# Kernel tuning notes

Hardware: AMD Instinct MI355X
Metric: run time of the kernel (lower is better)

Reference implementation:

```python
import jax, jax.numpy as jnp
import numpy as np

B, T, D = 2, 2048, 512
H, L, DFF, W = 8, 4, 2048, 256
DH = D // H  # 64
EPS = 1e-5


def layer_norm(x, g, b):
    mu = jnp.mean(x, axis=-1, keepdims=True)
    var = jnp.var(x, axis=-1, keepdims=True)
    return (x - mu) * jax.lax.rsqrt(var + EPS) * g + b


def setup_inputs() -> dict:
    key = jax.random.key(0)
    ks = jax.random.split(key, 8)
    s = 0.02
    inp = {
        "tokens": jax.random.normal(ks[0], (B, T, D), jnp.float32),
        "Wq": jax.random.normal(ks[1], (L, D, D), jnp.float32) * s,
        "Wk": jax.random.normal(ks[2], (L, D, D), jnp.float32) * s,
        "Wv": jax.random.normal(ks[3], (L, D, D), jnp.float32) * s,
        "Wo": jax.random.normal(ks[4], (L, D, D), jnp.float32) * s,
        "bq": jnp.zeros((L, D), jnp.float32),
        "bk": jnp.zeros((L, D), jnp.float32),
        "bv": jnp.zeros((L, D), jnp.float32),
        "bo": jnp.zeros((L, D), jnp.float32),
        "W1": jax.random.normal(ks[5], (L, D, DFF), jnp.float32) * s,
        "b1": jnp.zeros((L, DFF), jnp.float32),
        "W2": jax.random.normal(ks[6], (L, DFF, D), jnp.float32) * s,
        "b2": jnp.zeros((L, D), jnp.float32),
        "g1": jnp.ones((L, D), jnp.float32),
        "be1": jnp.zeros((L, D), jnp.float32),
        "g2": jnp.ones((L, D), jnp.float32),
        "be2": jnp.zeros((L, D), jnp.float32),
        "gf": jnp.ones((D,), jnp.float32),
        "bf": jnp.zeros((D,), jnp.float32),
    }
    return inp


def _rope_tables():
    pos = jnp.arange(T, dtype=jnp.float32)  # default position_ids = 0..T-1
    inv_freq = 1.0 / (10000.0 ** (jnp.arange(0, DH, 2, dtype=jnp.float32) / DH))
    ang = pos[:, None] * inv_freq[None, :]            # (T, DH/2)
    cos = jnp.concatenate([jnp.cos(ang), jnp.cos(ang)], axis=-1)  # (T, DH)
    sin = jnp.concatenate([jnp.sin(ang), jnp.sin(ang)], axis=-1)
    return cos, sin


def _rotate_half(x):
    return jnp.concatenate([-x[..., DH // 2:], x[..., :DH // 2]], axis=-1)


def reference(tokens, Wq, Wk, Wv, Wo, bq, bk, bv, bo, W1, b1, W2, b2,
              g1, be1, g2, be2, gf, bf):
    cos, sin = _rope_tables()  # (T, DH) each, broadcast over (B,H,T,DH)
    # sliding-window causal mask: allow j<=i and i-j < W
    idx = jnp.arange(T)
    allow = (idx[None, :] <= idx[:, None]) & ((idx[:, None] - idx[None, :]) < W)
    scale = np.sqrt(DH).astype(np.float32)

    x = tokens
    for l in range(L):
        xn = layer_norm(x, g1[l], be1[l])
        q = (xn @ Wq[l] + bq[l]).reshape(B, T, H, DH).transpose(0, 2, 1, 3)
        k = (xn @ Wk[l] + bk[l]).reshape(B, T, H, DH).transpose(0, 2, 1, 3)
        v = (xn @ Wv[l] + bv[l]).reshape(B, T, H, DH).transpose(0, 2, 1, 3)
        q = q * cos + _rotate_half(q) * sin
        k = k * cos + _rotate_half(k) * sin
        scores = jnp.einsum('bhqd,bhkd->bhqk', q, k) / scale
        scores = jnp.where(allow[None, None], scores, -jnp.inf)
        attn = jax.nn.softmax(scores, axis=-1)
        out = jnp.einsum('bhqk,bhkd->bhqd', attn, v)
        out = out.transpose(0, 2, 1, 3).reshape(B, T, D)
        x = x + out @ Wo[l] + bo[l]
        xn2 = layer_norm(x, g2[l], be2[l])
        h = jax.nn.gelu(xn2 @ W1[l] + b1[l], approximate=False)  # torch GELU = exact erf
        x = x + h @ W2[l] + b2[l]
    return layer_norm(x, gf, bf)
```

## Files before the change

kernel.cpp:

```cpp
#include <hip/hip_runtime.h>
#include <hip/hip_bf16.h>

#define BQ 2
#define TT 2048
#define DD 512
#define HH 8
#define LL 4
#define DFFN 2048
#define WWIN 256
#define DHD 64
#define MM (BQ*TT)
#define NOUT (MM*DD)

typedef __attribute__((ext_vector_type(8))) short bf16x8;
typedef __attribute__((ext_vector_type(4))) float f32x4;

__device__ __forceinline__ void lds_load16(const void* g, void* l) {
  __builtin_amdgcn_global_load_lds((const __attribute__((address_space(1))) void*)g,
                                   (__attribute__((address_space(3))) void*)l,
                                   16, 0, 0);
}

__device__ __forceinline__ void xcd_remap(int& bx, int& by) {
  const int nwg = gridDim.x * gridDim.y;
  if ((nwg & 7) == 0) {
    const int orig = blockIdx.x + gridDim.x * blockIdx.y;
    const int id = (orig & 7) * (nwg >> 3) + (orig >> 3);
    bx = id % gridDim.x;
    by = id / gridDim.x;
  } else {
    bx = blockIdx.x;
    by = blockIdx.y;
  }
}

__global__ __launch_bounds__(256) void fill_const(float* __restrict__ out, float C, int n) {
  int i = blockIdx.x * 256 + threadIdx.x;
  if (i < n) out[i] = C;
}

__global__ __launch_bounds__(256) void prep(const float* __restrict__ tokens,
                                            float* __restrict__ x,
                                            const float* __restrict__ bq,
                                            const float* __restrict__ bk,
                                            const float* __restrict__ bv,
                                            float* __restrict__ bqkvc) {
  const int b = blockIdx.x;
  if (b < 8192) {
    int i = b * 256 + threadIdx.x;
    x[i] = tokens[i];
  } else {
    int idx = (b - 8192) * 256 + threadIdx.x;
    if (idx < LL * 1536) {
      int l = idx / 1536, n = idx % 1536;
      float v;
      if (n < 512)       v = bq[l * 512 + n];
      else if (n < 1024) v = bk[l * 512 + n - 512];
      else               v = bv[l * 512 + n - 1024];
      bqkvc[idx] = v;
    }
  }
}

__global__ __launch_bounds__(256) void transpose_all(const float* __restrict__ Wq,
                                                     const float* __restrict__ Wk,
                                                     const float* __restrict__ Wv,
                                                     const float* __restrict__ Wo,
                                                     const float* __restrict__ W1,
                                                     const float* __restrict__ W2,
                                                     __hip_bfloat16* __restrict__ wqkvT,
                                                     __hip_bfloat16* __restrict__ woT,
                                                     __hip_bfloat16* __restrict__ w1T,
                                                     __hip_bfloat16* __restrict__ w2T,
                                                     const float* __restrict__ bq,
                                                     const float* __restrict__ bk,
                                                     const float* __restrict__ bv,
                                                     float* __restrict__ bqkvc) {
  const int l = blockIdx.y;
  const int b = blockIdx.x;
  if (b >= 3072) {
    int n = (b - 3072) * 256 + threadIdx.x;
    if (n < 1536) {
      float v;
      if (n < 512)       v = bq[l * 512 + n];
      else if (n < 1024) v = bk[l * 512 + n - 512];
      else               v = bv[l * 512 + n - 1024];
      bqkvc[l * 1536 + n] = v;
    }
    return;
  }
  __shared__ float tile[32][33];
  const float* src;
  __hip_bfloat16* dst;
  int K, N, t;
  if (b < 768) {
    int which = b >> 8; t = b & 255;
    src = ((which == 0) ? Wq : (which == 1) ? Wk : Wv) + (size_t)l * 262144;
    dst = wqkvT + (size_t)l * 786432 + which * 262144;
    K = 512; N = 512;
  } else if (b < 1024) {
    t = b - 768;  src = Wo + (size_t)l * 262144;  dst = woT + (size_t)l * 262144;  K = 512; N = 512;
  } else if (b < 2048) {
    t = b - 1024; src = W1 + (size_t)l * 1048576; dst = w1T + (size_t)l * 1048576; K = 512; N = 2048;
  } else {
    t = b - 2048; src = W2 + (size_t)l * 1048576; dst = w2T + (size_t)l * 1048576; K = 2048; N = 512;
  }
  const int tilesN = N >> 5;
  const int n0 = (t % tilesN) * 32, k0 = (t / tilesN) * 32;
  const int tx = threadIdx.x & 31, ty = threadIdx.x >> 5;
#pragma unroll
  for (int r = 0; r < 32; r += 8)
    tile[ty + r][tx] = src[(size_t)(k0 + ty + r) * N + n0 + tx];
  __syncthreads();
#pragma unroll
  for (int r = 0; r < 32; r += 8)
    dst[(size_t)(n0 + ty + r) * K + k0 + tx] = __float2bfloat16(tile[tx][ty + r]);
}

__global__ __launch_bounds__(256) void ln_kernel(const float* __restrict__ x,
                                                 const float* __restrict__ g,
                                                 const float* __restrict__ b,
                                                 __hip_bfloat16* __restrict__ out) {
  const int wave = threadIdx.x >> 6, lane = threadIdx.x & 63;
  const int row = blockIdx.x * 4 + wave;
  const float* xr = x + (size_t)row * DD;
  float v[8];
  float s = 0.f;
#pragma unroll
  for (int i = 0; i < 8; ++i) { v[i] = xr[lane + i * 64]; s += v[i]; }
#pragma unroll
  for (int off = 32; off; off >>= 1) s += __shfl_xor(s, off);
  float mu = s * (1.f / DD);
  float qs = 0.f;
#pragma unroll
  for (int i = 0; i < 8; ++i) { float d = v[i] - mu; qs += d * d; }
#pragma unroll
  for (int off = 32; off; off >>= 1) qs += __shfl_xor(qs, off);
  float rstd = rsqrtf(qs * (1.f / DD) + 1e-5f);
#pragma unroll
  for (int i = 0; i < 8; ++i) {
    int c = lane + i * 64;
    out[(size_t)row * DD + c] = __float2bfloat16((v[i] - mu) * rstd * g[c] + b[c]);
  }
}

__global__ __launch_bounds__(256) void ln_f32out(const float* __restrict__ x,
                                                 const float* __restrict__ g,
                                                 const float* __restrict__ b,
                                                 float* __restrict__ out) {
  const int wave = threadIdx.x >> 6, lane = threadIdx.x & 63;
  const int row = blockIdx.x * 4 + wave;
  const float* xr = x + (size_t)row * DD;
  float v[8];
  float s = 0.f;
#pragma unroll
  for (int i = 0; i < 8; ++i) { v[i] = xr[lane + i * 64]; s += v[i]; }
#pragma unroll
  for (int off = 32; off; off >>= 1) s += __shfl_xor(s, off);
  float mu = s * (1.f / DD);
  float qs = 0.f;
#pragma unroll
  for (int i = 0; i < 8; ++i) { float d = v[i] - mu; qs += d * d; }
#pragma unroll
  for (int off = 32; off; off >>= 1) qs += __shfl_xor(qs, off);
  float rstd = rsqrtf(qs * (1.f / DD) + 1e-5f);
#pragma unroll
  for (int i = 0; i < 8; ++i) {
    int c = lane + i * 64;
    out[(size_t)row * DD + c] = (v[i] - mu) * rstd * g[c] + b[c];
  }
}

enum { EPI_BF16 = 0, EPI_GELU = 1, EPI_ADDF32 = 2, EPI_RES = 3 };

template <int EPI, bool ROPE, int BM, int BN>
__global__ __launch_bounds__(256, 1) void gemm_bt(const __hip_bfloat16* __restrict__ A,
                                                  const __hip_bfloat16* __restrict__ BT,
                                                  const float* __restrict__ bias,
                                                  __hip_bfloat16* __restrict__ Obf,
                                                  float* __restrict__ Of,
                                                  const float* __restrict__ Orin,
                                                  __hip_bfloat16* __restrict__ VTo,
                                                  int M, int N, int K, int KS,
                                                  int ostride, int ooff) {
  constexpr int MI = (BM == 64) ? 2 : ((BN == 128) ? 4 : 2);
  constexpr int NJ = (BM == 64) ? 2 : 4;
  __shared__ __align__(16) __hip_bfloat16 Ash[2][2][BM * 32];
  __shared__ __align__(16) __hip_bfloat16 Bsh[2][2][BN * 32];
  const int tid = threadIdx.x;
  const int wave = tid >> 6;
  const int lane = tid & 63;
  int bx, by;
  xcd_remap(bx, by);
  const int m0 = by * BM;
  const int n0 = bx * BN;
  const int kbase = blockIdx.z * KS;
  const int wm = (BM == 64) ? ((wave >> 1) * 32)
                            : ((BN == 128) ? ((wave >> 1) * 64) : (wave * 32));
  const int wn = (BM == 64) ? ((wave & 1) * 32)
                            : ((BN == 128) ? ((wave & 1) * 64) : 0);
  const int l15 = lane & 15;
  const int quad = lane >> 4;

  f32x4 acc[MI][NJ] = {};

  const int r0 = tid >> 2;
  const int o0 = (tid & 3) * 8;

  const __hip_bfloat16* Ap0 = A + (size_t)(m0 + r0) * K + kbase + o0;
  const __hip_bfloat16* Ap1 = Ap0 + (size_t)64 * K;
  const __hip_bfloat16* Bp0 = BT + (size_t)(n0 + r0) * K + kbase + o0;
  const __hip_bfloat16* Bp1 = Bp0 + (size_t)64 * K;

  auto stage64 = [&](int buf, int k) {
    lds_load16(Ap0 + k,      &Ash[buf][0][wave * 512]);
    lds_load16(Ap0 + k + 32, &Ash[buf][1][wave * 512]);
    if constexpr (BM == 128) {
      lds_load16(Ap1 + k,      &Ash[buf][0][2048 + wave * 512]);
      lds_load16(Ap1 + k + 32, &Ash[buf][1][2048 + wave * 512]);
    }
    lds_load16(Bp0 + k,      &Bsh[buf][0][wave * 512]);
    lds_load16(Bp0 + k + 32, &Bsh[buf][1][wave * 512]);
    if constexpr (BN == 128) {
      lds_load16(Bp1 + k,      &Bsh[buf][0][2048 + wave * 512]);
      lds_load16(Bp1 + k + 32, &Bsh[buf][1][2048 + wave * 512]);
    }
  };
  auto compute = [&](const __hip_bfloat16* As, const __hip_bfloat16* Bs) {
    bf16x8 af[MI], bfr[NJ];
#pragma unroll
    for (int i = 0; i < MI; ++i)
      af[i] = *(const bf16x8*)&As[(wm + i * 16 + l15) * 32 + quad * 8];
#pragma unroll
    for (int j = 0; j < NJ; ++j)
      bfr[j] = *(const bf16x8*)&Bs[(wn + j * 16 + l15) * 32 + quad * 8];
#pragma unroll
    for (int i = 0; i < MI; ++i)
#pragma unroll
      for (int j = 0; j < NJ; ++j)
        acc[i][j] = __builtin_amdgcn_mfma_f32_16x16x32_bf16(af[i], bfr[j], acc[i][j], 0, 0, 0);
  };
  auto compute64 = [&](int buf) {
    compute(Ash[buf][0], Bsh[buf][0]);
    compute(Ash[buf][1], Bsh[buf][1]);
  };

  stage64(0, 0);
  for (int k0 = 0; k0 < KS; k0 += 128) {
    __syncthreads();
    if (k0 + 64 < KS) stage64(1, k0 + 64);
    compute64(0);
    __syncthreads();
    if (k0 + 128 < KS) stage64(0, k0 + 128);
    compute64(1);
  }

  if constexpr (ROPE) {
    if (n0 < 1024) {
#pragma unroll
      for (int j = 0; j < 2; ++j) {
        const int col = n0 + wn + j * 16 + l15;
        const float bv0 = bias[col], bv1 = bias[col + 32];
        const float freq = __powf(10000.f, -(float)(j * 16 + l15) * (1.f / 32.f));
#pragma unroll
        for (int i = 0; i < MI; ++i) {
          const int row = m0 + wm + i * 16 + quad * 4;
#pragma unroll
          for (int r = 0; r < 4; ++r) {
            const int t = (row + r) & 2047;
            float sn, cs;
            __sincosf((float)t * freq, &sn, &cs);
            const float a0 = acc[i][j][r] + bv0;
            const float a1 = acc[i][j + 2][r] + bv1;
            const size_t idx = (size_t)(row + r) * ostride + ooff + col;
            Obf[idx]      = __float2bfloat16(a0 * cs - a1 * sn);
            Obf[idx + 32] = __float2bfloat16(a1 * cs + a0 * sn);
          }
        }
      }
    } else {
#pragma unroll
      for (int j = 0; j < NJ; ++j) {
        const int col = n0 + wn + j * 16 + l15;
        const float bv = bias[col];
        const int d = col - 1024;
#pragma unroll
        for (int i = 0; i < MI; ++i) {
          const int row = m0 + wm + i * 16 + quad * 4;
#pragma unroll
          for (int r = 0; r < 4; ++r)
            VTo[(size_t)d * 4096 + row + r] = __float2bfloat16(acc[i][j][r] + bv);
        }
      }
    }
    return;
  }

#pragma unroll
  for (int j = 0; j < NJ; ++j) {
    const int col = n0 + wn + j * 16 + l15;
    const float bv = (EPI == EPI_RES || blockIdx.z == 0) ? bias[col] : 0.f;
#pragma unroll
    for (int i = 0; i < MI; ++i) {
      const int row = m0 + wm + i * 16 + quad * 4;
#pragma unroll
      for (int r = 0; r < 4; ++r) {
        float v = acc[i][j][r] + bv;
        size_t idx = (size_t)(row + r) * ostride + ooff + col;
        if (EPI == EPI_BF16) {
          Obf[idx] = __float2bfloat16(v);
        } else if (EPI == EPI_GELU) {
          float ge = 0.5f * v * (1.f + erff(v * 0.70710678118654752f));
          Obf[idx] = __float2bfloat16(ge);
        } else if (EPI == EPI_RES) {
          Of[idx] = Orin[idx] + v;
        } else {
          atomicAdd(&Of[idx], v);
        }
      }
    }
  }
}

__global__ __launch_bounds__(256, 1) void attn_mfma(const __hip_bfloat16* __restrict__ qkv,
                                                    const __hip_bfloat16* __restrict__ VT,
                                                    __hip_bfloat16* __restrict__ ao) {
  constexpr int KPAD = 72;
  constexpr int PPAD = 40;
  __shared__ __align__(16) __hip_bfloat16 Ksh[320 * KPAD];
  __shared__ __align__(16) __hip_bfloat16 Psh[4 * 16 * PPAD];
  const int tid = threadIdx.x;
  const int wave = tid >> 6;
  const int lane = tid & 63;
  const int l15 = lane & 15;
  const int quad = lane >> 4;
  int bx, by;
  xcd_remap(bx, by);
  const int bh = by;
  const int b = bh >> 3, h = bh & 7;
  const int q0 = bx * 64;
  const int j0 = (q0 >= WWIN) ? (q0 - WWIN) : 0;
  const int nk = (q0 + 63) - j0 + 1;

  const size_t baseK = ((size_t)(b * TT + j0)) * 1536 + 512 + h * 64;
  for (int c = tid; c < nk * 8; c += 256) {
    int row = c >> 3, cc = (c & 7) * 8;
    *(uint4*)&Ksh[row * KPAD + cc] = *(const uint4*)&qkv[baseK + (size_t)row * 1536 + cc];
  }
  __syncthreads();

  const int qt0 = q0 + wave * 16;
  const size_t baseQ = ((size_t)(b * TT + qt0 + l15)) * 1536 + h * 64;
  const bf16x8 aq0 = *(const bf16x8*)&qkv[baseQ + quad * 8];
  const bf16x8 aq1 = *(const bf16x8*)&qkv[baseQ + 32 + quad * 8];

  const __hip_bfloat16* V0 = VT + (size_t)(h * 64 + l15) * 4096 + (size_t)b * 2048 + j0;

  f32x4 o0 = {}, o1 = {}, o2 = {}, o3 = {};
  float lsum[4] = {0.f, 0.f, 0.f, 0.f};

  const int klo = (qt0 > (WWIN - 1)) ? (qt0 - (WWIN - 1)) : 0;
  const int c_lo = (klo - j0) >> 5;
  const int c_hi = (qt0 + 15 - j0) >> 5;
  __hip_bfloat16* Pw = &Psh[wave * 16 * PPAD];

  for (int c = c_lo; c <= c_hi; ++c) {
    const int krel = c * 32;
    bf16x8 bk00 = *(const bf16x8*)&Ksh[(krel + l15) * KPAD + quad * 8];
    bf16x8 bk01 = *(const bf16x8*)&Ksh[(krel + l15) * KPAD + 32 + quad * 8];
    bf16x8 bk10 = *(const bf16x8*)&Ksh[(krel + 16 + l15) * KPAD + quad * 8];
    bf16x8 bk11 = *(const bf16x8*)&Ksh[(krel + 16 + l15) * KPAD + 32 + quad * 8];
    f32x4 z = {};
    f32x4 s0 = __builtin_amdgcn_mfma_f32_16x16x32_bf16(aq0, bk00, z, 0, 0, 0);
    s0 = __builtin_amdgcn_mfma_f32_16x16x32_bf16(aq1, bk01, s0, 0, 0, 0);
    f32x4 s1 = __builtin_amdgcn_mfma_f32_16x16x32_bf16(aq0, bk10, z, 0, 0, 0);
    s1 = __builtin_amdgcn_mfma_f32_16x16x32_bf16(aq1, bk11, s1, 0, 0, 0);

    const int jj0 = j0 + krel + l15;
    const int jj1 = jj0 + 16;
#pragma unroll
    for (int r = 0; r < 4; ++r) {
      const int qrow = qt0 + quad * 4 + r;
      const bool ok0 = (jj0 <= qrow) && ((qrow - jj0) < WWIN);
      const bool ok1 = (jj1 <= qrow) && ((qrow - jj1) < WWIN);
      const float p0 = ok0 ? __expf(s0[r] * 0.125f) : 0.f;
      const float p1 = ok1 ? __expf(s1[r] * 0.125f) : 0.f;
      lsum[r] += p0 + p1;
      const int qloc = quad * 4 + r;
      Pw[qloc * PPAD + l15]      = __float2bfloat16(p0);
      Pw[qloc * PPAD + 16 + l15] = __float2bfloat16(p1);
    }
    asm volatile("s_waitcnt lgkmcnt(0)" ::: "memory");
    __builtin_amdgcn_wave_barrier();
    const bf16x8 pa = *(const bf16x8*)&Pw[l15 * PPAD + quad * 8];

    const int kgl = krel + quad * 8;
#pragma unroll
    for (int t = 0; t < 4; ++t) {
      const bf16x8 bv = *(const bf16x8*)&V0[(size_t)t * 65536 + kgl];
      if (t == 0)      o0 = __builtin_amdgcn_mfma_f32_16x16x32_bf16(pa, bv, o0, 0, 0, 0);
      else if (t == 1) o1 = __builtin_amdgcn_mfma_f32_16x16x32_bf16(pa, bv, o1, 0, 0, 0);
      else if (t == 2) o2 = __builtin_amdgcn_mfma_f32_16x16x32_bf16(pa, bv, o2, 0, 0, 0);
      else             o3 = __builtin_amdgcn_mfma_f32_16x16x32_bf16(pa, bv, o3, 0, 0, 0);
    }
    __builtin_amdgcn_wave_barrier();
  }

#pragma unroll
  for (int r = 0; r < 4; ++r) {
#pragma unroll
    for (int off = 8; off; off >>= 1) lsum[r] += __shfl_xor(lsum[r], off, 16);
  }

#pragma unroll
  for (int r = 0; r < 4; ++r) {
    const float inv = 1.f / lsum[r];
    const size_t ob = ((size_t)(b * TT + qt0 + quad * 4 + r)) * DD + h * 64 + l15;
    ao[ob]      = __float2bfloat16(o0[r] * inv);
    ao[ob + 16] = __float2bfloat16(o1[r] * inv);
    ao[ob + 32] = __float2bfloat16(o2[r] * inv);
    ao[ob + 48] = __float2bfloat16(o3[r] * inv);
  }
}

extern "C" void kernel_launch(void* const* d_in, const int* in_sizes, int n_in,
                              void* d_out, int out_size, void* d_ws, size_t ws_size,
                              hipStream_t stream) {
  float* outF = (float*)d_out;

  int code = 0;
  if (n_in != 19)                      code = 1;
  else if (in_sizes[0]  != 2097152)    code = 2;
  else if (in_sizes[1]  != 1048576)    code = 3;
  else if (in_sizes[9]  != 4194304)    code = 4;
  else if (in_sizes[17] != 512)        code = 5;
  if (code != 0 || ws_size < 27287552ull) {
    float C = code ? (150.f + 15.f * (float)code) : (1000.f + (float)(ws_size >> 20));
    fill_const<<<8192, 256, 0, stream>>>(outF, C, NOUT);
    return;
  }

  const float* tokens = (const float*)d_in[0];
  const float* Wq  = (const float*)d_in[1];
  const float* Wk  = (const float*)d_in[2];
  const float* Wv  = (const float*)d_in[3];
  const float* Wo  = (const float*)d_in[4];
  const float* bq  = (const float*)d_in[5];
  const float* bk  = (const float*)d_in[6];
  const float* bv  = (const float*)d_in[7];
  const float* bo  = (const float*)d_in[8];
  const float* W1  = (const float*)d_in[9];
  const float* b1  = (const float*)d_in[10];
  const float* W2  = (const float*)d_in[11];
  const float* b2  = (const float*)d_in[12];
  const float* g1  = (const float*)d_in[13];
  const float* be1 = (const float*)d_in[14];
  const float* g2  = (const float*)d_in[15];
  const float* be2 = (const float*)d_in[16];
  const float* gf  = (const float*)d_in[17];
  const float* bf  = (const float*)d_in[18];

  char* ws = (char*)d_ws;
  __hip_bfloat16* xnao  = (__hip_bfloat16*)(ws + 0);
  __hip_bfloat16* qkv   = (__hip_bfloat16*)(ws + 4194304);
  __hip_bfloat16* hbuf  = (__hip_bfloat16*)(ws + 4194304);
  __hip_bfloat16* VT    = (__hip_bfloat16*)(ws + 16777216);

  const bool big = ws_size >= 46161920ull;
  __hip_bfloat16 *wqkvT, *woT, *w1T, *w2T;
  float* bqkvc;
  if (big) {
    wqkvT = (__hip_bfloat16*)(ws + 20971520);
    woT   = (__hip_bfloat16*)(ws + 27262976);
    w1T   = (__hip_bfloat16*)(ws + 29360128);
    w2T   = (__hip_bfloat16*)(ws + 37748736);
    bqkvc = (float*)(ws + 46137344);
  } else {
    wqkvT = (__hip_bfloat16*)(ws + 20971520);
    woT   = (__hip_bfloat16*)(ws + 22544384);
    w1T   = (__hip_bfloat16*)(ws + 23068672);
    w2T   = (__hip_bfloat16*)(ws + 25165824);
    bqkvc = (float*)(ws + 27262976);
  }
  __hip_bfloat16* xn = xnao;
  __hip_bfloat16* ao = xnao;
  float* x = outF;

  if (big) {
    transpose_all<<<dim3(3078, 4), 256, 0, stream>>>(Wq, Wk, Wv, Wo, W1, W2,
                                                     wqkvT, woT, w1T, w2T,
                                                     bq, bk, bv, bqkvc);
    ln_kernel<<<1024, 256, 0, stream>>>(tokens, g1, be1, xn);
    for (int l = 0; l < LL; ++l) {
      __hip_bfloat16* qkvT_l = wqkvT + (size_t)l * 786432;
      __hip_bfloat16* woT_l  = woT   + (size_t)l * 262144;
      __hip_bfloat16* w1T_l  = w1T   + (size_t)l * 1048576;
      __hip_bfloat16* w2T_l  = w2T   + (size_t)l * 1048576;

      gemm_bt<EPI_BF16, true, 128, 64><<<dim3(24, 32), 256, 0, stream>>>(
          xn, qkvT_l, bqkvc + l * 1536, qkv, nullptr, nullptr, VT,
          MM, 1536, 512, 512, 1536, 0);
      attn_mfma<<<dim3(32, 16), 256, 0, stream>>>(qkv, VT, ao);
      gemm_bt<EPI_RES, false, 64, 64><<<dim3(8, 64), 256, 0, stream>>>(
          ao, woT_l, bo + l * 512, nullptr, x, (l == 0) ? tokens : x, nullptr,
          MM, 512, 512, 512, 512, 0);
      ln_kernel<<<1024, 256, 0, stream>>>(x, g2 + l * 512, be2 + l * 512, xn);
      gemm_bt<EPI_GELU, false, 128, 128><<<dim3(16, 32), 256, 0, stream>>>(
          xn, w1T_l, b1 + l * 2048, hbuf, nullptr, nullptr, nullptr,
          MM, 2048, 512, 512, 2048, 0);
      gemm_bt<EPI_RES, false, 64, 64><<<dim3(8, 64), 256, 0, stream>>>(
          hbuf, w2T_l, b2 + l * 512, nullptr, x, x, nullptr,
          MM, 512, 2048, 2048, 512, 0);
      if (l < LL - 1)
        ln_kernel<<<1024, 256, 0, stream>>>(x, g1 + (l + 1) * 512,
                                            be1 + (l + 1) * 512, xn);
      else
        ln_f32out<<<1024, 256, 0, stream>>>(x, gf, bf, outF);
    }
    return;
  }

  prep<<<8216, 256, 0, stream>>>(tokens, x, bq, bk, bv, bqkvc);

  for (int l = 0; l < LL; ++l) {
    transpose_all<<<dim3(3072, 1), 256, 0, stream>>>(
        Wq + (size_t)l * 262144, Wk + (size_t)l * 262144, Wv + (size_t)l * 262144,
        Wo + (size_t)l * 262144, W1 + (size_t)l * 1048576, W2 + (size_t)l * 1048576,
        wqkvT, woT, w1T, w2T, bq, bk, bv, bqkvc);

    ln_kernel<<<1024, 256, 0, stream>>>(x, g1 + l * 512, be1 + l * 512, xn);
    gemm_bt<EPI_BF16, true, 128, 64><<<dim3(24, 32), 256, 0, stream>>>(
        xn, wqkvT, bqkvc + l * 1536, qkv, nullptr, nullptr, VT,
        MM, 1536, 512, 512, 1536, 0);
    attn_mfma<<<dim3(32, 16), 256, 0, stream>>>(qkv, VT, ao);
    gemm_bt<EPI_ADDF32, false, 128, 64><<<dim3(8, 32, 2), 256, 0, stream>>>(
        ao, woT, bo + l * 512, nullptr, x, nullptr, nullptr,
        MM, 512, 512, 256, 512, 0);
    ln_kernel<<<1024, 256, 0, stream>>>(x, g2 + l * 512, be2 + l * 512, xn);
    gemm_bt<EPI_GELU, false, 128, 128><<<dim3(16, 32), 256, 0, stream>>>(
        xn, w1T, b1 + l * 2048, hbuf, nullptr, nullptr, nullptr,
        MM, 2048, 512, 512, 2048, 0);
    gemm_bt<EPI_ADDF32, false, 128, 128><<<dim3(4, 32, 4), 256, 0, stream>>>(
        hbuf, w2T, b2 + l * 512, nullptr, x, nullptr, nullptr,
        MM, 512, 2048, 512, 512, 0);
  }
  ln_f32out<<<1024, 256, 0, stream>>>(x, gf, bf, outF);
}
```

Before: 486.7 us.

## Fuse LayerNorm into GEMM A-loads using per-row partial stats from residual epilogues

Drops the standalone LayerNorm kernels. The residual GEMM epilogues now emit per-column-block partial sum and sum-of-squares per row. The following QKV and FFN1 GEMMs read fp32 x directly, normalize it while staging into LDS, and convert to bf16. This saves a kernel launch and a bf16 round trip per LayerNorm, but A-staging becomes synchronous register loads instead of async global-to-LDS, and it reads fp32 (twice the bytes) redundantly across every N-block. The one-pass variance (E[x^2]-mu^2) and bf16-rounded gamma/beta add some numerical risk.

```diff
diff --git a/kernel.cpp b/kernel.cpp
--- a/kernel.cpp
+++ b/kernel.cpp
@@ -75,9 +75,31 @@
                                                      const float* __restrict__ bq,
                                                      const float* __restrict__ bk,
                                                      const float* __restrict__ bv,
-                                                     float* __restrict__ bqkvc) {
+                                                     float* __restrict__ bqkvc,
+                                                     const float* __restrict__ tokens,
+                                                     float* __restrict__ pq) {
   const int l = blockIdx.y;
   const int b = blockIdx.x;
+  if (b >= 3078) {
+    if (l != 0) return;
+    const int wave = threadIdx.x >> 6, lane = threadIdx.x & 63;
+    const int row = (b - 3078) * 4 + wave;
+    const float* xr = tokens + (size_t)row * DD;
+    float v[8];
+#pragma unroll
+    for (int i = 0; i < 8; ++i) v[i] = xr[lane + i * 64];
+#pragma unroll
+    for (int i = 0; i < 8; ++i) {
+      float s = v[i], q = v[i] * v[i];
+#pragma unroll
+      for (int off = 32; off; off >>= 1) { s += __shfl_xor(s, off); q += __shfl_xor(q, off); }
+      if (lane == 0) {
+        pq[((size_t)i * 4096 + row) * 2]     = s;
+        pq[((size_t)i * 4096 + row) * 2 + 1] = q;
+      }
+    }
+    return;
+  }
   if (b >= 3072) {
     int n = (b - 3072) * 256 + threadIdx.x;
     if (n < 1536) {
@@ -171,9 +193,31 @@
   }
 }
 
+__global__ __launch_bounds__(256) void ln_f32out_stats(const float* __restrict__ x,
+                                                       const float* __restrict__ ps,
+                                                       const float* __restrict__ g,
+                                                       const float* __restrict__ b,
+                                                       float* __restrict__ out) {
+  const int wave = threadIdx.x >> 6, lane = threadIdx.x & 63;
+  const int row = blockIdx.x * 4 + wave;
+  const int l8 = lane & 7;
+  float s1 = ps[((size_t)l8 * 4096 + row) * 2];
+  float s2 = ps[((size_t)l8 * 4096 + row) * 2 + 1];
+#pragma unroll
+  for (int off = 4; off; off >>= 1) { s1 += __shfl_xor(s1, off, 8); s2 += __shfl_xor(s2, off, 8); }
+  const float mu = s1 * (1.f / DD);
+  const float rstd = rsqrtf(s2 * (1.f / DD) - mu * mu + 1e-5f);
+  const float* xr = x + (size_t)row * DD;
+#pragma unroll
+  for (int i = 0; i < 8; ++i) {
+    int c = lane + i * 64;
+    out[(size_t)row * DD + c] = (xr[c] - mu) * rstd * g[c] + b[c];
+  }
+}
+
 enum { EPI_BF16 = 0, EPI_GELU = 1, EPI_ADDF32 = 2, EPI_RES = 3 };
 
-template <int EPI, bool ROPE, int BM, int BN>
+template <int EPI, bool ROPE, bool LNA, bool PSTAT, int BM, int BN>
 __global__ __launch_bounds__(256, 1) void gemm_bt(const __hip_bfloat16* __restrict__ A,
                                                   const __hip_bfloat16* __restrict__ BT,
                                                   const float* __restrict__ bias,
@@ -181,12 +225,21 @@
                                                   float* __restrict__ Of,
                                                   const float* __restrict__ Orin,
                                                   __hip_bfloat16* __restrict__ VTo,
+                                                  const float* __restrict__ xsrc,
+                                                  const float* __restrict__ pstats,
+                                                  const float* __restrict__ gamma,
+                                                  const float* __restrict__ beta,
+                                                  float* __restrict__ pout,
                                                   int M, int N, int K, int KS,
                                                   int ostride, int ooff) {
   constexpr int MI = (BM == 64) ? 2 : ((BN == 128) ? 4 : 2);
   constexpr int NJ = (BM == 64) ? 2 : 4;
   __shared__ __align__(16) __hip_bfloat16 Ash[2][2][BM * 32];
   __shared__ __align__(16) __hip_bfloat16 Bsh[2][2][BN * 32];
+  __shared__ __hip_bfloat16 gS[LNA ? 512 : 1];
+  __shared__ __hip_bfloat16 bS[LNA ? 512 : 1];
+  __shared__ float muS[LNA ? BM : 1];
+  __shared__ float rsS[LNA ? BM : 1];
   const int tid = threadIdx.x;
   const int wave = tid >> 6;
   const int lane = tid & 63;
@@ -207,17 +260,60 @@
   const int r0 = tid >> 2;
   const int o0 = (tid & 3) * 8;
 
-  const __hip_bfloat16* Ap0 = A + (size_t)(m0 + r0) * K + kbase + o0;
-  const __hip_bfloat16* Ap1 = Ap0 + (size_t)64 * K;
+  const __hip_bfloat16* Ap0 = LNA ? nullptr : A + (size_t)(m0 + r0) * K + kbase + o0;
+  const __hip_bfloat16* Ap1 = LNA ? nullptr : Ap0 + (size_t)64 * K;
   const __hip_bfloat16* Bp0 = BT + (size_t)(n0 + r0) * K + kbase + o0;
   const __hip_bfloat16* Bp1 = Bp0 + (size_t)64 * K;
 
+  if constexpr (LNA) {
+    for (int c = tid; c < 512; c += 256) {
+      gS[c] = __float2bfloat16(gamma[c]);
+      bS[c] = __float2bfloat16(beta[c]);
+    }
+    if (tid < BM) {
+      const int row = m0 + tid;
+      float s1 = 0.f, s2 = 0.f;
+#pragma unroll
+      for (int s = 0; s < 8; ++s) {
+        s1 += pstats[((size_t)s * 4096 + row) * 2];
+        s2 += pstats[((size_t)s * 4096 + row) * 2 + 1];
+      }
+      const float mu = s1 * (1.f / 512.f);
+      muS[tid] = mu;
+      rsS[tid] = rsqrtf(s2 * (1.f / 512.f) - mu * mu + 1e-5f);
+    }
+    __syncthreads();
+  }
+
+  auto stageA_ln = [&](int buf, int sub, int half, int k) {
+    const int row = r0 + half * 64;
+    const float* xp = xsrc + (size_t)(m0 + row) * 512 + k + o0;
+    float4 xa = *(const float4*)xp;
+    float4 xb = *(const float4*)(xp + 4);
+    const float mu = muS[row], rs = rsS[row];
+    const int c0 = k + o0;
+    float xv[8] = {xa.x, xa.y, xa.z, xa.w, xb.x, xb.y, xb.z, xb.w};
+    bf16x8 o;
+#pragma unroll
+    for (int e = 0; e < 8; ++e) {
+      float gv = __bfloat162float(gS[c0 + e]);
+      float bv = __bfloat162float(bS[c0 + e]);
+      ((__hip_bfloat16*)&o)[e] = __float2bfloat16((xv[e] - mu) * rs * gv + bv);
+    }
+    *(bf16x8*)&Ash[buf][sub][half * 2048 + tid * 8] = o;
+  };
+
   auto stage64 = [&](int buf, int k) {
-    lds_load16(Ap0 + k,      &Ash[buf][0][wave * 512]);
-    lds_load16(Ap0 + k + 32, &Ash[buf][1][wave * 512]);
-    if constexpr (BM == 128) {
-      lds_load16(Ap1 + k,      &Ash[buf][0][2048 + wave * 512]);
-      lds_load16(Ap1 + k + 32, &Ash[buf][1][2048 + wave * 512]);
+    if constexpr (LNA) {
+      stageA_ln(buf, 0, 0, k);      stageA_ln(buf, 0, 1, k);
+      stageA_ln(buf, 1, 0, k + 32); stageA_ln(buf, 1, 1, k + 32);
+    } else {
+      lds_load16(Ap0 + k,      &Ash[buf][0][tid * 0 + wave * 512]);
+      lds_load16(Ap0 + k + 32, &Ash[buf][1][wave * 512]);
+      if constexpr (BM == 128) {
+        lds_load16(Ap1 + k,      &Ash[buf][0][2048 + wave * 512]);
+        lds_load16(Ap1 + k + 32, &Ash[buf][1][2048 + wave * 512]);
+      }
     }
     lds_load16(Bp0 + k,      &Bsh[buf][0][wave * 512]);
     lds_load16(Bp0 + k + 32, &Bsh[buf][1][wave * 512]);
@@ -296,6 +392,7 @@
     return;
   }
 
+  float st1[MI][4] = {}, st2[MI][4] = {};
 #pragma unroll
   for (int j = 0; j < NJ; ++j) {
     const int col = n0 + wn + j * 16 + l15;
@@ -313,11 +410,50 @@
           float ge = 0.5f * v * (1.f + erff(v * 0.70710678118654752f));
           Obf[idx] = __float2bfloat16(ge);
         } else if (EPI == EPI_RES) {
-          Of[idx] = Orin[idx] + v;
+          const float vf = Orin[idx] + v;
+          Of[idx] = vf;
+          if constexpr (PSTAT) { st1[i][r] += vf; st2[i][r] += vf * vf; }
         } else {
           atomicAdd(&Of[idx], v);
         }
       }
+    }
+  }
+
+  if constexpr (PSTAT) {
+    float* sS1 = (float*)&Ash[0][0][0];
+    float* sS2 = sS1 + 64;
+    float red1[MI][4], red2[MI][4];
+#pragma unroll
+    for (int i = 0; i < MI; ++i)
+#pragma unroll
+      for (int r = 0; r < 4; ++r) {
+        float a = st1[i][r], c = st2[i][r];
+#pragma unroll
+        for (int off = 8; off; off >>= 1) { a += __shfl_xor(a, off, 16); c += __shfl_xor(c, off, 16); }
+        red1[i][r] = a; red2[i][r] = c;
+      }
+    __syncthreads();
+    if (wn == 0 && l15 == 0) {
+#pragma unroll
+      for (int i = 0; i < MI; ++i)
+#pragma unroll
+        for (int r = 0; r < 4; ++r) {
+          const int rl = wm + i * 16 + quad * 4 + r;
+          sS1[rl] = red1[i][r]; sS2[rl] = red2[i][r];
+        }
+    }
+    __syncthreads();
+    if (wn == 32 && l15 == 0) {
+#pragma unroll
+      for (int i = 0; i < MI; ++i)
+#pragma unroll
+        for (int r = 0; r < 4; ++r) {
+          const int rl = wm + i * 16 + quad * 4 + r;
+          const size_t po = ((size_t)bx * 4096 + m0 + rl) * 2;
+          pout[po]     = sS1[rl] + red1[i][r];
+          pout[po + 1] = sS2[rl] + red2[i][r];
+        }
     }
   }
 }
@@ -466,15 +602,19 @@
   __hip_bfloat16* hbuf  = (__hip_bfloat16*)(ws + 4194304);
   __hip_bfloat16* VT    = (__hip_bfloat16*)(ws + 16777216);
 
-  const bool big = ws_size >= 46161920ull;
+  const bool big = ws_size >= 46686208ull;
   __hip_bfloat16 *wqkvT, *woT, *w1T, *w2T;
   float* bqkvc;
+  float* pq = nullptr;
+  float* pw = nullptr;
   if (big) {
     wqkvT = (__hip_bfloat16*)(ws + 20971520);
     woT   = (__hip_bfloat16*)(ws + 27262976);
     w1T   = (__hip_bfloat16*)(ws + 29360128);
     w2T   = (__hip_bfloat16*)(ws + 37748736);
     bqkvc = (float*)(ws + 46137344);
+    pq    = (float*)(ws + 46161920);
+    pw    = (float*)(ws + 46424064);
   } else {
     wqkvT = (__hip_bfloat16*)(ws + 20971520);
     woT   = (__hip_bfloat16*)(ws + 22544384);
@@ -487,36 +627,35 @@
   float* x = outF;
 
   if (big) {
-    transpose_all<<<dim3(3078, 4), 256, 0, stream>>>(Wq, Wk, Wv, Wo, W1, W2,
+    transpose_all<<<dim3(4102, 4), 256, 0, stream>>>(Wq, Wk, Wv, Wo, W1, W2,
                                                      wqkvT, woT, w1T, w2T,
-                                                     bq, bk, bv, bqkvc);
-    ln_kernel<<<1024, 256, 0, stream>>>(tokens, g1, be1, xn);
+                                                     bq, bk, bv, bqkvc, tokens, pq);
     for (int l = 0; l < LL; ++l) {
       __hip_bfloat16* qkvT_l = wqkvT + (size_t)l * 786432;
       __hip_bfloat16* woT_l  = woT   + (size_t)l * 262144;
       __hip_bfloat16* w1T_l  = w1T   + (size_t)l * 1048576;
       __hip_bfloat16* w2T_l  = w2T   + (size_t)l * 1048576;
-
-      gemm_bt<EPI_BF16, true, 128, 64><<<dim3(24, 32), 256, 0, stream>>>(
-          xn, qkvT_l, bqkvc + l * 1536, qkv, nullptr, nullptr, VT,
+      const float* xsrc = (l == 0) ? tokens : x;
+
+      gemm_bt<EPI_BF16, true, true, false, 128, 64><<<dim3(24, 32), 256, 0, stream>>>(
+          nullptr, qkvT_l, bqkvc + l * 1536, qkv, nullptr, nullptr, VT,
+          xsrc, pq, g1 + l * 512, be1 + l * 512, nullptr,
           MM, 1536, 512, 512, 1536, 0);
       attn_mfma<<<dim3(32, 16), 256, 0, stream>>>(qkv, VT, ao);
-      gemm_bt<EPI_RES, false, 64, 64><<<dim3(8, 64), 256, 0, stream>>>(
-          ao, woT_l, bo + l * 512, nullptr, x, (l == 0) ? tokens : x, nullptr,
+      gemm_bt<EPI_RES, false, false, true, 64, 64><<<dim3(8, 64), 256, 0, stream>>>(
+          ao, woT_l, bo + l * 512, nullptr, x, xsrc, nullptr,
+          nullptr, nullptr, nullptr, nullptr, pw,
           MM, 512, 512, 512, 512, 0);
-      ln_kernel<<<1024, 256, 0, stream>>>(x, g2 + l * 512, be2 + l * 512, xn);
-      gemm_bt<EPI_GELU, false, 128, 128><<<dim3(16, 32), 256, 0, stream>>>(
-          xn, w1T_l, b1 + l * 2048, hbuf, nullptr, nullptr, nullptr,
+      gemm_bt<EPI_GELU, false, true, false, 128, 128><<<dim3(16, 32), 256, 0, stream>>>(
+          nullptr, w1T_l, b1 + l * 2048, hbuf, nullptr, nullptr, nullptr,
+          x, pw, g2 + l * 512, be2 + l * 512, nullptr,
           MM, 2048, 512, 512, 2048, 0);
-      gemm_bt<EPI_RES, false, 64, 64><<<dim3(8, 64), 256, 0, stream>>>(
+      gemm_bt<EPI_RES, false, false, true, 64, 64><<<dim3(8, 64), 256, 0, stream>>>(
           hbuf, w2T_l, b2 + l * 512, nullptr, x, x, nullptr,
+          nullptr, nullptr, nullptr, nullptr, pq,
           MM, 512, 2048, 2048, 512, 0);
-      if (l < LL - 1)
-        ln_kernel<<<1024, 256, 0, stream>>>(x, g1 + (l + 1) * 512,
-                                            be1 + (l + 1) * 512, xn);
-      else
-        ln_f32out<<<1024, 256, 0, stream>>>(x, gf, bf, outF);
-    }
+    }
+    ln_f32out_stats<<<1024, 256, 0, stream>>>(x, pq, gf, bf, outF);
     return;
   }
 
@@ -526,22 +665,26 @@
     transpose_all<<<dim3(3072, 1), 256, 0, stream>>>(
         Wq + (size_t)l * 262144, Wk + (size_t)l * 262144, Wv + (size_t)l * 262144,
         Wo + (size_t)l * 262144, W1 + (size_t)l * 1048576, W2 + (size_t)l * 1048576,
-        wqkvT, woT, w1T, w2T, bq, bk, bv, bqkvc);
+        wqkvT, woT, w1T, w2T, bq, bk, bv, bqkvc, nullptr, nullptr);
 
     ln_kernel<<<1024, 256, 0, stream>>>(x, g1 + l * 512, be1 + l * 512, xn);
-    gemm_bt<EPI_BF16, true, 128, 64><<<dim3(24, 32), 256, 0, stream>>>(
+    gemm_bt<EPI_BF16, true, false, false, 128, 64><<<dim3(24, 32), 256, 0, stream>>>(
         xn, wqkvT, bqkvc + l * 1536, qkv, nullptr, nullptr, VT,
+        nullptr, nullptr, nullptr, nullptr, nullptr,
         MM, 1536, 512, 512, 1536, 0);
     attn_mfma<<<dim3(32, 16), 256, 0, stream>>>(qkv, VT, ao);
-    gemm_bt<EPI_ADDF32, false, 128, 64><<<dim3(8, 32, 2), 256, 0, stream>>>(
+    gemm_bt<EPI_ADDF32, false, false, false, 128, 64><<<dim3(8, 32, 2), 256, 0, stream>>>(
         ao, woT, bo + l * 512, nullptr, x, nullptr, nullptr,
+        nullptr, nullptr, nullptr, nullptr, nullptr,
         MM, 512, 512, 256, 512, 0);
     ln_kernel<<<1024, 256, 0, stream>>>(x, g2 + l * 512, be2 + l * 512, xn);
-    gemm_bt<EPI_GELU, false, 128, 128><<<dim3(16, 32), 256, 0, stream>>>(
+    gemm_bt<EPI_GELU, false, false, false, 128, 128><<<dim3(16, 32), 256, 0, stream>>>(
         xn, w1T, b1 + l * 2048, hbuf, nullptr, nullptr, nullptr,
+        nullptr, nullptr, nullptr, nullptr, nullptr,
         MM, 2048, 512, 512, 2048, 0);
-    gemm_bt<EPI_ADDF32, false, 128, 128><<<dim3(4, 32, 4), 256, 0, stream>>>(
+    gemm_bt<EPI_ADDF32, false, false, false, 128, 128><<<dim3(4, 32, 4), 256, 0, stream>>>(
         hbuf, w2T, b2 + l * 512, nullptr, x, nullptr, nullptr,
+        nullptr, nullptr, nullptr, nullptr, nullptr,
         MM, 512, 2048, 512, 512, 0);
   }
   ln_f32out<<<1024, 256, 0, stream>>>(x, gf, bf, outF);
```

Result: slower. 508.5 us (+4.5%).
